# Kernel optimization log

Measured on AMD Instinct MI355X. Metric: run time of the kernel, lower is better.

The kernel has to match this reference:

```python
import jax, jax.numpy as jnp
import numpy as np

B, T, D, K = 4, 4096, 384, 64

def setup_inputs() -> dict:
    key = jax.random.key(0)
    k1, k2, k3, k4 = jax.random.split(key, 4)
    x = jax.random.normal(k1, (B, T, D), dtype=jnp.float32)
    # nn.Linear weights stored as (out_features, in_features); y = x @ W.T
    Wk = jax.random.normal(k2, (K, D), dtype=jnp.float32) * (1.0 / np.sqrt(D))
    Wq = jax.random.normal(k3, (K, D), dtype=jnp.float32) * (1.0 / np.sqrt(D))
    Wv = jax.random.normal(k4, (D, D), dtype=jnp.float32) * (1.0 / np.sqrt(D))
    return {"x": x, "Wk": Wk, "Wq": Wq, "Wv": Wv}

def reference(x, Wk, Wq, Wv):
    # x: (B,T,D)
    k = jnp.einsum('btd,kd->btk', x, Wk)   # (B,T,K)
    q = jnp.einsum('btd,kd->btk', x, Wq)   # (B,T,K)
    v = jnp.einsum('btd,ed->bte', x, Wv)   # (B,T,D)
    scores = jnp.einsum('btk,bsk->bts', q, k)  # (B,T,T)
    Tq = x.shape[1]
    causal = jnp.tril(jnp.ones((Tq, Tq), dtype=bool))[None, :, :]
    scores = jnp.where(causal, scores, -jnp.inf)
    w = jax.nn.softmax(scores / jnp.sqrt(jnp.asarray(Wk.shape[0], scores.dtype)), axis=-1)
    return jnp.einsum('bts,bsd->btd', w, v)  # (B,T,D)
```

## Files before the change

kernel.cpp:

```cpp
#include <hip/hip_runtime.h>


#define BB 4
#define TT 4096
#define DD 384

#define OWKA 0
#define OWQA 24576
#define OWVB 49152
#define OYK  196608
#define OYQ  1245184
#define OVT  2293760

#define C_EXP 0.18033688011112042f

typedef __bf16 bf16x8 __attribute__((ext_vector_type(8)));
typedef float f32x16 __attribute__((ext_vector_type(16)));
typedef unsigned short u16x4 __attribute__((ext_vector_type(4)));

__device__ __forceinline__ unsigned short f2bf(float f) {
  unsigned int u = __builtin_bit_cast(unsigned int, f);
  u += 0x7FFFu + ((u >> 16) & 1u);
  return (unsigned short)(u >> 16);
}

__device__ __forceinline__ bf16x8 ldb8(const unsigned short* p) {
  return *reinterpret_cast<const bf16x8*>(p);
}

__global__ __launch_bounds__(256) void convert_w(
    const float* __restrict__ Wk, const float* __restrict__ Wq,
    const float* __restrict__ Wv, unsigned short* __restrict__ ws) {
  int g = blockIdx.x * 256 + threadIdx.x;
  int row = g / 96;
  int fin = (g - row * 96) * 4;
  const float* src;
  unsigned short* dstbase;
  int m;
  if (row < 64)       { src = Wk + row * 384;         dstbase = ws + OWKA; m = row; }
  else if (row < 128) { src = Wq + (row - 64) * 384;  dstbase = ws + OWQA; m = row - 64; }
  else                { src = Wv + (row - 128) * 384; dstbase = ws + OWVB; m = row - 128; }
  float4 f = *reinterpret_cast<const float4*>(src + fin);
  u16x4 o;
  o[0] = f2bf(f.x); o[1] = f2bf(f.y); o[2] = f2bf(f.z); o[3] = f2bf(f.w);
  unsigned short* dst = dstbase + (m >> 5) * 12288 + (fin >> 4) * 512
                        + ((((fin >> 3) & 1) << 5) + (m & 31)) * 8 + (fin & 7);
  *reinterpret_cast<u16x4*>(dst) = o;
}

__global__ __launch_bounds__(512) void proj_fused(
    const float* __restrict__ x, const unsigned short* __restrict__ ws_r,
    unsigned short* __restrict__ Yk, unsigned short* __restrict__ Yq,
    unsigned short* __restrict__ Vt) {
  __shared__ __align__(16) unsigned short xlds[24576];
  int tb = blockIdx.x;
  int b = tb >> 6;
  int tid = threadIdx.x;
  {
    int r = tid >> 3, e = tid & 7;
    const float* xr = x + (tb * 64 + r) * DD + e * 48;
#pragma unroll
    for (int i = 0; i < 12; i++) {
      int fin = e * 48 + i * 4;
      float4 f = *reinterpret_cast<const float4*>(xr + i * 4);
      u16x4 o;
      o[0] = f2bf(f.x); o[1] = f2bf(f.y); o[2] = f2bf(f.z); o[3] = f2bf(f.w);
      unsigned short* dst = xlds + (r >> 5) * 12288 + (fin >> 4) * 512
                            + ((((fin >> 3) & 1) << 5) + (r & 31)) * 8 + (fin & 7);
      *reinterpret_cast<u16x4*>(dst) = o;
    }
  }
  __syncthreads();
  int wid = tid >> 6, lane = tid & 63;
  int l31 = lane & 31, h8 = lane >> 5;
  const f32x16 fz16 = {};
  if (wid < 2) {
    const unsigned short* Wa = ws_r + (wid ? OWQA : OWKA) + lane * 8;
    unsigned short* Ysel = (wid ? Yq : Yk);
    f32x16 acc[2][2];
    acc[0][0] = fz16; acc[0][1] = fz16; acc[1][0] = fz16; acc[1][1] = fz16;
    for (int ks = 0; ks < 24; ks++) {
      bf16x8 a0 = ldb8(Wa + ks * 512);
      bf16x8 a1 = ldb8(Wa + 12288 + ks * 512);
      bf16x8 b0 = ldb8(xlds + ks * 512 + lane * 8);
      bf16x8 b1 = ldb8(xlds + 12288 + ks * 512 + lane * 8);
      acc[0][0] = __builtin_amdgcn_mfma_f32_32x32x16_bf16(a0, b0, acc[0][0], 0, 0, 0);
      acc[0][1] = __builtin_amdgcn_mfma_f32_32x32x16_bf16(a0, b1, acc[0][1], 0, 0, 0);
      acc[1][0] = __builtin_amdgcn_mfma_f32_32x32x16_bf16(a1, b0, acc[1][0], 0, 0, 0);
      acc[1][1] = __builtin_amdgcn_mfma_f32_32x32x16_bf16(a1, b1, acc[1][1], 0, 0, 0);
    }
#pragma unroll
    for (int mt = 0; mt < 2; mt++)
#pragma unroll
      for (int nt = 0; nt < 2; nt++) {
        int tile = b * 128 + (tb & 63) * 2 + nt;
#pragma unroll
        for (int rg = 0; rg < 4; rg++) {
          u16x4 o;
#pragma unroll
          for (int i = 0; i < 4; i++) o[i] = f2bf(acc[mt][nt][rg * 4 + i]);
          *reinterpret_cast<u16x4*>(Ysel + tile * 2048 + (mt * 2 + (rg >> 1)) * 512
                                    + (((rg & 1) << 5) + l31) * 8 + 4 * h8) = o;
        }
      }
  } else {
    int vw = wid - 2;
    const unsigned short* Wb = ws_r + OWVB + vw * 2 * 12288 + lane * 8;
    f32x16 acc[2][2];
    acc[0][0] = fz16; acc[0][1] = fz16; acc[1][0] = fz16; acc[1][1] = fz16;
    for (int ks = 0; ks < 24; ks++) {
      bf16x8 a0 = ldb8(xlds + ks * 512 + lane * 8);
      bf16x8 a1 = ldb8(xlds + 12288 + ks * 512 + lane * 8);
      bf16x8 w0 = ldb8(Wb + ks * 512);
      bf16x8 w1 = ldb8(Wb + 12288 + ks * 512);
      acc[0][0] = __builtin_amdgcn_mfma_f32_32x32x16_bf16(a0, w0, acc[0][0], 0, 0, 0);
      acc[0][1] = __builtin_amdgcn_mfma_f32_32x32x16_bf16(a0, w1, acc[0][1], 0, 0, 0);
      acc[1][0] = __builtin_amdgcn_mfma_f32_32x32x16_bf16(a1, w0, acc[1][0], 0, 0, 0);
      acc[1][1] = __builtin_amdgcn_mfma_f32_32x32x16_bf16(a1, w1, acc[1][1], 0, 0, 0);
    }
    int k128 = (tb & 63) >> 1;
#pragma unroll
    for (int t32 = 0; t32 < 2; t32++)
#pragma unroll
      for (int dt = 0; dt < 2; dt++) {
        int dti = vw * 2 + dt;
        unsigned short* vbase = Vt + ((b * 12 + dti) * 32 + k128) * 4096;
#pragma unroll
        for (int rg = 0; rg < 4; rg++) {
          u16x4 o;
#pragma unroll
          for (int i = 0; i < 4; i++) o[i] = f2bf(acc[t32][dt][rg * 4 + i]);
          int kseg = 4 * (tb & 1) + t32 * 2 + (rg >> 1);
          *reinterpret_cast<u16x4*>(vbase + kseg * 512
                                    + (((rg & 1) << 5) + l31) * 8 + 4 * h8) = o;
        }
      }
  }
}

__global__ __launch_bounds__(256, 2) void flash_attn(
    const unsigned short* __restrict__ Yk, const unsigned short* __restrict__ Yq,
    const unsigned short* __restrict__ Vt, float* __restrict__ out) {
  __shared__ __align__(16) unsigned short pbuf[2][8192];
  __shared__ float lred[4][32];
  int blk = blockIdx.x;
  int xcd = blk & 7;
  int b = xcd >> 1, half = xcd & 1;
  int n = blk >> 3;
  int st = (n < 32) ? (127 - 2 * n - half) : (2 * (n - 32) + half);
  int wid = threadIdx.x >> 6, lane = threadIdx.x & 63;
  int l31 = lane & 31, h8 = lane >> 5;
  const f32x16 fz16 = {};
  const unsigned short* qbase = Yq + (b * 128 + st) * 2048 + lane * 8;
  bf16x8 qf[4];
#pragma unroll
  for (int ks = 0; ks < 4; ks++) qf[ks] = ldb8(qbase + ks * 512);
  f32x16 acc[3];
  acc[0] = fz16; acc[1] = fz16; acc[2] = fz16;
  float psum = 0.f;
  int n128 = (st >> 2) + 1;
  int qrow = st * 32 + l31;
  const unsigned short* kbase = Yk + (b * 128 + wid) * 2048 + lane * 8;
  const unsigned short* vbase = Vt + ((b * 12 + wid * 3) * 32) * 4096 + lane * 8;
#pragma unroll 1
  for (int kb = 0; kb < n128; kb++) {
    const unsigned short* kt = kbase + kb * 8192;
    bf16x8 kf[4];
#pragma unroll
    for (int ks = 0; ks < 4; ks++) kf[ks] = ldb8(kt + ks * 512);
    f32x16 sacc = fz16;
#pragma unroll
    for (int ks = 0; ks < 4; ks++)
      sacc = __builtin_amdgcn_mfma_f32_32x32x16_bf16(kf[ks], qf[ks], sacc, 0, 0, 0);
    int kg0 = kb * 128 + wid * 32 + 4 * h8;
    unsigned short* pw = pbuf[kb & 1];
#pragma unroll
    for (int rg = 0; rg < 4; rg++) {
      u16x4 o;
#pragma unroll
      for (int i = 0; i < 4; i++) {
        int key = kg0 + rg * 8 + i;
        float pv = (key > qrow) ? 0.f : exp2f(sacc[rg * 4 + i] * C_EXP);
        psum += pv;
        o[i] = f2bf(pv);
      }
      int g = wid * 2 + (rg >> 1);
      *reinterpret_cast<u16x4*>(pw + g * 512 + ((rg & 1) * 32 + l31) * 8 + 4 * h8) = o;
    }
    const unsigned short* vt = vbase + kb * 4096;
    bf16x8 vf0[8], vf1[8], vf2[8];
#pragma unroll
    for (int g = 0; g < 8; g++) vf0[g] = ldb8(vt + g * 512);
#pragma unroll
    for (int g = 0; g < 8; g++) vf1[g] = ldb8(vt + 32 * 4096 + g * 512);
#pragma unroll
    for (int g = 0; g < 8; g++) vf2[g] = ldb8(vt + 64 * 4096 + g * 512);
    __syncthreads();
    bf16x8 pf[8];
#pragma unroll
    for (int g = 0; g < 8; g++) pf[g] = ldb8(pw + g * 512 + lane * 8);
#pragma unroll
    for (int g = 0; g < 8; g++) {
      acc[0] = __builtin_amdgcn_mfma_f32_32x32x16_bf16(vf0[g], pf[g], acc[0], 0, 0, 0);
      acc[1] = __builtin_amdgcn_mfma_f32_32x32x16_bf16(vf1[g], pf[g], acc[1], 0, 0, 0);
      acc[2] = __builtin_amdgcn_mfma_f32_32x32x16_bf16(vf2[g], pf[g], acc[2], 0, 0, 0);
    }
  }
  psum += __shfl_xor(psum, 32);
  if (h8 == 0) lred[wid][l31] = psum;
  __syncthreads();
  float lt = lred[0][l31] + lred[1][l31] + lred[2][l31] + lred[3][l31];
  float inv = 1.0f / lt;
  float* ob = out + (b * TT + st * 32 + l31) * DD + wid * 96;
#pragma unroll
  for (int dt = 0; dt < 3; dt++)
#pragma unroll
    for (int rg = 0; rg < 4; rg++) {
      float4 o4;
      o4.x = acc[dt][rg * 4 + 0] * inv; o4.y = acc[dt][rg * 4 + 1] * inv;
      o4.z = acc[dt][rg * 4 + 2] * inv; o4.w = acc[dt][rg * 4 + 3] * inv;
      *reinterpret_cast<float4*>(ob + dt * 32 + rg * 8 + h8 * 4) = o4;
    }
}

extern "C" void kernel_launch(void* const* d_in, const int* in_sizes, int n_in,
                              void* d_out, int out_size, void* d_ws, size_t ws_size,
                              hipStream_t stream) {
  const float* x  = (const float*)d_in[0];
  const float* Wk = (const float*)d_in[1];
  const float* Wq = (const float*)d_in[2];
  const float* Wv = (const float*)d_in[3];
  unsigned short* ws = (unsigned short*)d_ws;
  unsigned short* Yk = ws + OYK;
  unsigned short* Yq = ws + OYQ;
  unsigned short* Vt = ws + OVT;

  convert_w<<<192, 256, 0, stream>>>(Wk, Wq, Wv, ws);
  proj_fused<<<256, 512, 0, stream>>>(x, ws, Yk, Yq, Vt);
  flash_attn<<<512, 256, 0, stream>>>(Yk, Yq, Vt, (float*)d_out);
}
```

Baseline: 152.7 us.

## Split key blocks across two wave groups per attention block with LDS reduction

Each flash-attention block now runs 512 threads as two groups of four waves. The groups take alternating 128-key tiles, and the second group's partial accumulators and row sums are combined with the first group's through shared memory at the end. The goal is to halve the serial key loop per query tile, which shortens the long causal rows and adds latency hiding. In exchange there is an extra LDS reduction pass, a padded final iteration that is fully masked when the tile count is odd, and tighter register limits from the raised launch bounds, which could cause spills.

```diff
diff --git a/kernel.cpp b/kernel.cpp
--- a/kernel.cpp
+++ b/kernel.cpp
@@ -138,17 +138,18 @@
   }
 }
 
-__global__ __launch_bounds__(256, 2) void flash_attn(
+__global__ __launch_bounds__(512, 4) void flash_attn(
     const unsigned short* __restrict__ Yk, const unsigned short* __restrict__ Yq,
     const unsigned short* __restrict__ Vt, float* __restrict__ out) {
-  __shared__ __align__(16) unsigned short pbuf[2][8192];
-  __shared__ float lred[4][32];
+  __shared__ __align__(16) unsigned short pbuf[2][2][8192];
   int blk = blockIdx.x;
   int xcd = blk & 7;
   int b = xcd >> 1, half = xcd & 1;
   int n = blk >> 3;
   int st = (n < 32) ? (127 - 2 * n - half) : (2 * (n - 32) + half);
-  int wid = threadIdx.x >> 6, lane = threadIdx.x & 63;
+  int tid = threadIdx.x;
+  int wid = tid >> 6, lane = tid & 63;
+  int g = wid >> 2, wg = wid & 3;
   int l31 = lane & 31, h8 = lane >> 5;
   const f32x16 fz16 = {};
   const unsigned short* qbase = Yq + (b * 128 + st) * 2048 + lane * 8;
@@ -159,12 +160,15 @@
   acc[0] = fz16; acc[1] = fz16; acc[2] = fz16;
   float psum = 0.f;
   int n128 = (st >> 2) + 1;
+  int W = (n128 + 1) >> 1;
   int qrow = st * 32 + l31;
-  const unsigned short* kbase = Yk + (b * 128 + wid) * 2048 + lane * 8;
-  const unsigned short* vbase = Vt + ((b * 12 + wid * 3) * 32) * 4096 + lane * 8;
+  const unsigned short* kbase = Yk + (b * 128 + wg) * 2048 + lane * 8;
+  const unsigned short* vbase = Vt + ((b * 12 + wg * 3) * 32) * 4096 + lane * 8;
 #pragma unroll 1
-  for (int kb = 0; kb < n128; kb++) {
-    const unsigned short* kt = kbase + kb * 8192;
+  for (int it = 0; it < W; it++) {
+    int kb = 2 * it + g;
+    int kbc = (kb < n128) ? kb : (n128 - 1);
+    const unsigned short* kt = kbase + kbc * 8192;
     bf16x8 kf[4];
 #pragma unroll
     for (int ks = 0; ks < 4; ks++) kf[ks] = ldb8(kt + ks * 512);
@@ -172,8 +176,8 @@
 #pragma unroll
     for (int ks = 0; ks < 4; ks++)
       sacc = __builtin_amdgcn_mfma_f32_32x32x16_bf16(kf[ks], qf[ks], sacc, 0, 0, 0);
-    int kg0 = kb * 128 + wid * 32 + 4 * h8;
-    unsigned short* pw = pbuf[kb & 1];
+    int kg0 = kb * 128 + wg * 32 + 4 * h8;
+    unsigned short* pw = pbuf[g][it & 1];
 #pragma unroll
     for (int rg = 0; rg < 4; rg++) {
       u16x4 o;
@@ -184,43 +188,58 @@
         psum += pv;
         o[i] = f2bf(pv);
       }
-      int g = wid * 2 + (rg >> 1);
-      *reinterpret_cast<u16x4*>(pw + g * 512 + ((rg & 1) * 32 + l31) * 8 + 4 * h8) = o;
-    }
-    const unsigned short* vt = vbase + kb * 4096;
+      int gq = wg * 2 + (rg >> 1);
+      *reinterpret_cast<u16x4*>(pw + gq * 512 + ((rg & 1) * 32 + l31) * 8 + 4 * h8) = o;
+    }
+    const unsigned short* vt = vbase + kbc * 4096;
     bf16x8 vf0[8], vf1[8], vf2[8];
 #pragma unroll
-    for (int g = 0; g < 8; g++) vf0[g] = ldb8(vt + g * 512);
-#pragma unroll
-    for (int g = 0; g < 8; g++) vf1[g] = ldb8(vt + 32 * 4096 + g * 512);
-#pragma unroll
-    for (int g = 0; g < 8; g++) vf2[g] = ldb8(vt + 64 * 4096 + g * 512);
+    for (int q = 0; q < 8; q++) vf0[q] = ldb8(vt + q * 512);
+#pragma unroll
+    for (int q = 0; q < 8; q++) vf1[q] = ldb8(vt + 32 * 4096 + q * 512);
+#pragma unroll
+    for (int q = 0; q < 8; q++) vf2[q] = ldb8(vt + 64 * 4096 + q * 512);
     __syncthreads();
     bf16x8 pf[8];
 #pragma unroll
-    for (int g = 0; g < 8; g++) pf[g] = ldb8(pw + g * 512 + lane * 8);
-#pragma unroll
-    for (int g = 0; g < 8; g++) {
-      acc[0] = __builtin_amdgcn_mfma_f32_32x32x16_bf16(vf0[g], pf[g], acc[0], 0, 0, 0);
-      acc[1] = __builtin_amdgcn_mfma_f32_32x32x16_bf16(vf1[g], pf[g], acc[1], 0, 0, 0);
-      acc[2] = __builtin_amdgcn_mfma_f32_32x32x16_bf16(vf2[g], pf[g], acc[2], 0, 0, 0);
+    for (int q = 0; q < 8; q++) pf[q] = ldb8(pw + q * 512 + lane * 8);
+#pragma unroll
+    for (int q = 0; q < 8; q++) {
+      acc[0] = __builtin_amdgcn_mfma_f32_32x32x16_bf16(vf0[q], pf[q], acc[0], 0, 0, 0);
+      acc[1] = __builtin_amdgcn_mfma_f32_32x32x16_bf16(vf1[q], pf[q], acc[1], 0, 0, 0);
+      acc[2] = __builtin_amdgcn_mfma_f32_32x32x16_bf16(vf2[q], pf[q], acc[2], 0, 0, 0);
     }
   }
   psum += __shfl_xor(psum, 32);
-  if (h8 == 0) lred[wid][l31] = psum;
   __syncthreads();
-  float lt = lred[0][l31] + lred[1][l31] + lred[2][l31] + lred[3][l31];
-  float inv = 1.0f / lt;
-  float* ob = out + (b * TT + st * 32 + l31) * DD + wid * 96;
-#pragma unroll
-  for (int dt = 0; dt < 3; dt++)
-#pragma unroll
-    for (int rg = 0; rg < 4; rg++) {
-      float4 o4;
-      o4.x = acc[dt][rg * 4 + 0] * inv; o4.y = acc[dt][rg * 4 + 1] * inv;
-      o4.z = acc[dt][rg * 4 + 2] * inv; o4.w = acc[dt][rg * 4 + 3] * inv;
-      *reinterpret_cast<float4*>(ob + dt * 32 + rg * 8 + h8 * 4) = o4;
-    }
+  float* fb = reinterpret_cast<float*>(pbuf);
+  if (h8 == 0) fb[12288 + wid * 32 + l31] = psum;
+  if (g == 1) {
+#pragma unroll
+    for (int dt = 0; dt < 3; dt++)
+#pragma unroll
+      for (int e = 0; e < 16; e++)
+        fb[wg * 3072 + (dt * 16 + e) * 64 + lane] = acc[dt][e];
+  }
+  __syncthreads();
+  if (g == 0) {
+    float lt = 0.f;
+#pragma unroll
+    for (int w = 0; w < 8; w++) lt += fb[12288 + w * 32 + l31];
+    float inv = 1.0f / lt;
+    float* ob = out + (b * TT + st * 32 + l31) * DD + wg * 96;
+#pragma unroll
+    for (int dt = 0; dt < 3; dt++)
+#pragma unroll
+      for (int rg = 0; rg < 4; rg++) {
+        float4 o4;
+        o4.x = (acc[dt][rg * 4 + 0] + fb[wg * 3072 + (dt * 16 + rg * 4 + 0) * 64 + lane]) * inv;
+        o4.y = (acc[dt][rg * 4 + 1] + fb[wg * 3072 + (dt * 16 + rg * 4 + 1) * 64 + lane]) * inv;
+        o4.z = (acc[dt][rg * 4 + 2] + fb[wg * 3072 + (dt * 16 + rg * 4 + 2) * 64 + lane]) * inv;
+        o4.w = (acc[dt][rg * 4 + 3] + fb[wg * 3072 + (dt * 16 + rg * 4 + 3) * 64 + lane]) * inv;
+        *reinterpret_cast<float4*>(ob + dt * 32 + rg * 8 + h8 * 4) = o4;
+      }
+  }
 }
 
 extern "C" void kernel_launch(void* const* d_in, const int* in_sizes, int n_in,
@@ -237,5 +256,5 @@
 
   convert_w<<<192, 256, 0, stream>>>(Wk, Wq, Wv, ws);
   proj_fused<<<256, 512, 0, stream>>>(x, ws, Yk, Yq, Vt);
-  flash_attn<<<512, 256, 0, stream>>>(Yk, Yq, Vt, (float*)d_out);
-}
+  flash_attn<<<512, 512, 0, stream>>>(Yk, Yq, Vt, (float*)d_out);
+}
```

Measured after the change: 422.1 us. +176.5%, slower.
